# Kernel optimization log

Measured on AMD Instinct MI355X. Metric: run time of the kernel, lower is better.

Reference implementation:

```python
import jax, jax.numpy as jnp
import numpy as np

B, N, H, E = 8, 256, 128, 32

def setup_inputs() -> dict:
    key = jax.random.key(0)
    ks = jax.random.split(key, 9)
    x = jax.random.normal(ks[0], (B, N, H), dtype=jnp.float32)
    adj = jax.random.randint(ks[1], (B, N, N), 0, 2, dtype=jnp.int32)
    e = jax.random.normal(ks[2], (B, N, N, E), dtype=jnp.float32)
    s = 0.02
    We = jax.random.normal(ks[3], (E, H), dtype=jnp.float32) * s
    be = jax.random.normal(ks[4], (H,), dtype=jnp.float32) * s
    W1 = jax.random.normal(ks[5], (H, 2 * H), dtype=jnp.float32) * s
    b1 = jax.random.normal(ks[6], (2 * H,), dtype=jnp.float32) * s
    W2 = jax.random.normal(ks[7], (2 * H, H), dtype=jnp.float32) * s
    b2 = jax.random.normal(ks[8], (H,), dtype=jnp.float32) * s
    return {"x": x, "adj": adj, "e": e, "We": We, "be": be,
            "W1": W1, "b1": b1, "W2": W2, "b2": b2}

def reference(x, adj, e, We, be, W1, b1, W2, b2):
    # edge projection: [B,N,N,E] -> [B,N,N,H]
    e_h = jnp.einsum('bije,eh->bijh', e, We) + be
    # message m[b,i,j] = relu(x[b,j] + e_h[b,i,j]); mask by adj
    m = jax.nn.relu(x[:, None, :, :] + e_h)
    m = jnp.where((adj != 0)[..., None], m, jnp.zeros((), m.dtype))
    agg = m.sum(axis=2)  # sum over j -> [B,N,H]
    h = agg + x
    out = jax.nn.relu(h @ W1 + b1) @ W2 + b2
    return out
```

## Files before the change

### kernel.cpp

```cpp
#include <hip/hip_runtime.h>
#include <hip/hip_bf16.h>

#define B_ 8
#define N_ 256
#define H_ 128
#define E_ 32

typedef __bf16 bf16x8 __attribute__((ext_vector_type(8)));
typedef float f32x4 __attribute__((ext_vector_type(4)));

static __device__ __forceinline__ __bf16 f2bf(float f) {
    union { float f; unsigned int u; } a;
    a.f = f;
    const unsigned int r = a.u + 0x7FFFu + ((a.u >> 16) & 1u);
    union { unsigned short s; __bf16 b; } o;
    o.s = (unsigned short)(r >> 16);
    return o.b;
}

__global__ __launch_bounds__(256, 2) void fused_kernel(
    const float* __restrict__ x, const int* __restrict__ adj,
    const float* __restrict__ e, const float* __restrict__ We,
    const float* __restrict__ be, const float* __restrict__ W1,
    const float* __restrict__ b1, const float* __restrict__ W2,
    const float* __restrict__ b2, float* __restrict__ out)
{
    __shared__ float red[4][128];
    __shared__ float hvec[128];
    __shared__ float ts[256];
    __shared__ float part[256];

    const int bi   = blockIdx.x;
    const int b    = bi >> 8;
    const int tid  = threadIdx.x;
    const int w    = tid >> 6;
    const int lane = tid & 63;
    const int quad = lane >> 4;
    const int col  = lane & 15;

    bf16x8 bw[8];
    float  bef[8];
#pragma unroll
    for (int ht = 0; ht < 8; ++ht) {
#pragma unroll
        for (int kk = 0; kk < 8; ++kk)
            bw[ht][kk] = f2bf(We[(quad * 8 + kk) * H_ + ht * 16 + col]);
        bef[ht] = be[ht * 16 + col];
    }

    float psum[8];
#pragma unroll
    for (int ht = 0; ht < 8; ++ht) psum[ht] = 0.0f;

    const size_t ebase   = (size_t)bi * (N_ * E_);
    const size_t adjbase = (size_t)bi * N_;
    const f32x4 zero4 = {0.0f, 0.0f, 0.0f, 0.0f};

#pragma unroll
    for (int c = 0; c < 4; ++c) {
        const int j0 = (c * 4 + w) * 16;

        const float* ap = e + ebase + (size_t)(j0 + col) * E_ + quad * 8;
        const float4 a0 = *(const float4*)ap;
        const float4 a1 = *(const float4*)(ap + 4);
        bf16x8 af;
        af[0] = f2bf(a0.x); af[1] = f2bf(a0.y); af[2] = f2bf(a0.z); af[3] = f2bf(a0.w);
        af[4] = f2bf(a1.x); af[5] = f2bf(a1.y); af[6] = f2bf(a1.z); af[7] = f2bf(a1.w);

        float adjf[4];
        const int jr = j0 + quad * 4;
#pragma unroll
        for (int r = 0; r < 4; ++r)
            adjf[r] = adj[adjbase + jr + r] ? 1.0f : 0.0f;

        const float* xrow = x + ((size_t)(b * N_ + jr)) * H_ + col;

#pragma unroll
        for (int g = 0; g < 2; ++g) {
            f32x4 acc[4];
#pragma unroll
            for (int t = 0; t < 4; ++t)
                acc[t] = __builtin_amdgcn_mfma_f32_16x16x32_bf16(af, bw[g * 4 + t], zero4, 0, 0, 0);
#pragma unroll
            for (int r = 0; r < 4; ++r) {
                const float* xr = xrow + (size_t)r * H_;
#pragma unroll
                for (int t = 0; t < 4; ++t) {
                    const int ht = g * 4 + t;
                    const float v = acc[t][r] + xr[ht * 16] + bef[ht];
                    psum[ht] += adjf[r] * fmaxf(v, 0.0f);
                }
            }
        }
    }

#pragma unroll
    for (int ht = 0; ht < 8; ++ht) {
        float v = psum[ht];
        v += __shfl_xor(v, 16);
        v += __shfl_xor(v, 32);
        if (lane < 16) red[w][ht * 16 + lane] = v;
    }
    __syncthreads();
    if (tid < 128) {
        const float aggv = red[0][tid] + red[1][tid] + red[2][tid] + red[3][tid];
        hvec[tid] = aggv + x[(size_t)bi * H_ + tid];
    }
    __syncthreads();

    {
        const int c = tid;
        float a0 = 0.f, a1 = 0.f, a2 = 0.f, a3 = 0.f;
        for (int k = 0; k < 128; k += 4) {
            a0 += hvec[k + 0] * W1[(k + 0) * 256 + c];
            a1 += hvec[k + 1] * W1[(k + 1) * 256 + c];
            a2 += hvec[k + 2] * W1[(k + 2) * 256 + c];
            a3 += hvec[k + 3] * W1[(k + 3) * 256 + c];
        }
        ts[c] = fmaxf((a0 + a1) + (a2 + a3) + b1[c], 0.0f);
    }
    __syncthreads();

    {
        const int c    = tid & 127;
        const int kb   = (tid >> 7) * 128;
        float a0 = 0.f, a1 = 0.f, a2 = 0.f, a3 = 0.f;
        for (int k = 0; k < 128; k += 4) {
            a0 += ts[kb + k + 0] * W2[(kb + k + 0) * 128 + c];
            a1 += ts[kb + k + 1] * W2[(kb + k + 1) * 128 + c];
            a2 += ts[kb + k + 2] * W2[(kb + k + 2) * 128 + c];
            a3 += ts[kb + k + 3] * W2[(kb + k + 3) * 128 + c];
        }
        part[tid] = (a0 + a1) + (a2 + a3);
    }
    __syncthreads();
    if (tid < 128)
        out[(size_t)bi * H_ + tid] = part[tid] + part[tid + 128] + b2[tid];
}

extern "C" void kernel_launch(void* const* d_in, const int* in_sizes, int n_in,
                              void* d_out, int out_size, void* d_ws, size_t ws_size,
                              hipStream_t stream) {
    const float* x   = (const float*)d_in[0];
    const int*   adj = (const int*)  d_in[1];
    const float* e   = (const float*)d_in[2];
    const float* We  = (const float*)d_in[3];
    const float* be  = (const float*)d_in[4];
    const float* W1  = (const float*)d_in[5];
    const float* b1  = (const float*)d_in[6];
    const float* W2  = (const float*)d_in[7];
    const float* b2  = (const float*)d_in[8];
    float* out = (float*)d_out;

    fused_kernel<<<dim3(B_ * N_), dim3(256), 0, stream>>>(
        x, adj, e, We, be, W1, b1, W2, b2, out);
}
```

Measured before the change: 167.0 us.

## Process four nodes per block, stage x tiles in LDS, batch MLP

```diff
diff --git a/kernel.cpp b/kernel.cpp
--- a/kernel.cpp
+++ b/kernel.cpp
@@ -5,6 +5,7 @@
 #define N_ 256
 #define H_ 128
 #define E_ 32
+#define XS_STRIDE 132
 
 typedef __bf16 bf16x8 __attribute__((ext_vector_type(8)));
 typedef float f32x4 __attribute__((ext_vector_type(4)));
@@ -25,13 +26,15 @@
     const float* __restrict__ b1, const float* __restrict__ W2,
     const float* __restrict__ b2, float* __restrict__ out)
 {
-    __shared__ float red[4][128];
-    __shared__ float hvec[128];
-    __shared__ float ts[256];
-    __shared__ float part[256];
-
-    const int bi   = blockIdx.x;
-    const int b    = bi >> 8;
+    __shared__ float xs[4][16 * XS_STRIDE];
+    __shared__ float red[4][2][128];
+    __shared__ float hvec[4][128];
+    __shared__ float ts[4][256];
+    __shared__ float part[4][256];
+
+    const int tile = blockIdx.x;
+    const int b    = tile >> 6;
+    const int i0   = (tile & 63) << 2;
     const int tid  = threadIdx.x;
     const int w    = tid >> 6;
     const int lane = tid & 63;
@@ -48,94 +51,141 @@
         bef[ht] = be[ht * 16 + col];
     }
 
-    float psum[8];
-#pragma unroll
-    for (int ht = 0; ht < 8; ++ht) psum[ht] = 0.0f;
-
-    const size_t ebase   = (size_t)bi * (N_ * E_);
-    const size_t adjbase = (size_t)bi * N_;
     const f32x4 zero4 = {0.0f, 0.0f, 0.0f, 0.0f};
 
-#pragma unroll
-    for (int c = 0; c < 4; ++c) {
-        const int j0 = (c * 4 + w) * 16;
-
-        const float* ap = e + ebase + (size_t)(j0 + col) * E_ + quad * 8;
-        const float4 a0 = *(const float4*)ap;
-        const float4 a1 = *(const float4*)(ap + 4);
-        bf16x8 af;
-        af[0] = f2bf(a0.x); af[1] = f2bf(a0.y); af[2] = f2bf(a0.z); af[3] = f2bf(a0.w);
-        af[4] = f2bf(a1.x); af[5] = f2bf(a1.y); af[6] = f2bf(a1.z); af[7] = f2bf(a1.w);
-
-        float adjf[4];
-        const int jr = j0 + quad * 4;
-#pragma unroll
-        for (int r = 0; r < 4; ++r)
-            adjf[r] = adj[adjbase + jr + r] ? 1.0f : 0.0f;
-
-        const float* xrow = x + ((size_t)(b * N_ + jr)) * H_ + col;
-
-#pragma unroll
-        for (int g = 0; g < 2; ++g) {
-            f32x4 acc[4];
-#pragma unroll
-            for (int t = 0; t < 4; ++t)
-                acc[t] = __builtin_amdgcn_mfma_f32_16x16x32_bf16(af, bw[g * 4 + t], zero4, 0, 0, 0);
-#pragma unroll
-            for (int r = 0; r < 4; ++r) {
-                const float* xr = xrow + (size_t)r * H_;
-#pragma unroll
-                for (int t = 0; t < 4; ++t) {
-                    const int ht = g * 4 + t;
-                    const float v = acc[t][r] + xr[ht * 16] + bef[ht];
-                    psum[ht] += adjf[r] * fmaxf(v, 0.0f);
+    for (int pass = 0; pass < 2; ++pass) {
+        const int ia = i0 + pass * 2;
+
+        float psum[2][8];
+#pragma unroll
+        for (int ii = 0; ii < 2; ++ii)
+#pragma unroll
+            for (int ht = 0; ht < 8; ++ht) psum[ii][ht] = 0.0f;
+
+#pragma unroll
+        for (int c = 0; c < 4; ++c) {
+            const int j0 = (c * 4 + w) * 16;
+
+            {
+                const float* src = x + ((size_t)(b * N_ + j0)) * H_;
+#pragma unroll
+                for (int q = 0; q < 8; ++q) {
+                    const int idx = q * 64 + lane;
+                    const int row = idx >> 5, c4 = idx & 31;
+                    const float4 v = *(const float4*)(src + (size_t)idx * 4);
+                    *(float4*)&xs[w][row * XS_STRIDE + c4 * 4] = v;
                 }
             }
-        }
-    }
-
-#pragma unroll
-    for (int ht = 0; ht < 8; ++ht) {
-        float v = psum[ht];
-        v += __shfl_xor(v, 16);
-        v += __shfl_xor(v, 32);
-        if (lane < 16) red[w][ht * 16 + lane] = v;
-    }
-    __syncthreads();
-    if (tid < 128) {
-        const float aggv = red[0][tid] + red[1][tid] + red[2][tid] + red[3][tid];
-        hvec[tid] = aggv + x[(size_t)bi * H_ + tid];
-    }
-    __syncthreads();
+
+            const int jr = j0 + quad * 4;
+
+#pragma unroll
+            for (int ii = 0; ii < 2; ++ii) {
+                const int i = ia + ii;
+                const size_t rowbase = (size_t)(b * N_ + i) * N_;
+
+                const int4 av = *(const int4*)(adj + rowbase + jr);
+                float adjf[4];
+                adjf[0] = av.x ? 1.0f : 0.0f;
+                adjf[1] = av.y ? 1.0f : 0.0f;
+                adjf[2] = av.z ? 1.0f : 0.0f;
+                adjf[3] = av.w ? 1.0f : 0.0f;
+
+                const float* ap = e + (rowbase + (size_t)(j0 + col)) * E_ + quad * 8;
+                const float4 a0 = *(const float4*)ap;
+                const float4 a1 = *(const float4*)(ap + 4);
+                bf16x8 af;
+                af[0] = f2bf(a0.x); af[1] = f2bf(a0.y); af[2] = f2bf(a0.z); af[3] = f2bf(a0.w);
+                af[4] = f2bf(a1.x); af[5] = f2bf(a1.y); af[6] = f2bf(a1.z); af[7] = f2bf(a1.w);
+
+#pragma unroll
+                for (int g = 0; g < 2; ++g) {
+                    f32x4 acc[4];
+#pragma unroll
+                    for (int t = 0; t < 4; ++t)
+                        acc[t] = __builtin_amdgcn_mfma_f32_16x16x32_bf16(af, bw[g * 4 + t], zero4, 0, 0, 0);
+#pragma unroll
+                    for (int r = 0; r < 4; ++r) {
+                        const float* xr = &xs[w][(quad * 4 + r) * XS_STRIDE + col];
+#pragma unroll
+                        for (int t = 0; t < 4; ++t) {
+                            const int ht = g * 4 + t;
+                            const float v = acc[t][r] + xr[ht * 16] + bef[ht];
+                            psum[ii][ht] += adjf[r] * fmaxf(v, 0.0f);
+                        }
+                    }
+                }
+            }
+        }
+
+#pragma unroll
+        for (int ii = 0; ii < 2; ++ii)
+#pragma unroll
+            for (int ht = 0; ht < 8; ++ht) {
+                float v = psum[ii][ht];
+                v += __shfl_xor(v, 16);
+                v += __shfl_xor(v, 32);
+                if (lane < 16) red[w][ii][ht * 16 + lane] = v;
+            }
+        __syncthreads();
+        {
+            const int g = tid >> 7, t = tid & 127;
+            const float aggv = red[0][g][t] + red[1][g][t] + red[2][g][t] + red[3][g][t];
+            hvec[pass * 2 + g][t] = aggv + x[((size_t)(b * N_ + ia + g)) * H_ + t];
+        }
+        __syncthreads();
+    }
 
     {
         const int c = tid;
-        float a0 = 0.f, a1 = 0.f, a2 = 0.f, a3 = 0.f;
+        float acc[4] = {0.f, 0.f, 0.f, 0.f};
         for (int k = 0; k < 128; k += 4) {
-            a0 += hvec[k + 0] * W1[(k + 0) * 256 + c];
-            a1 += hvec[k + 1] * W1[(k + 1) * 256 + c];
-            a2 += hvec[k + 2] * W1[(k + 2) * 256 + c];
-            a3 += hvec[k + 3] * W1[(k + 3) * 256 + c];
-        }
-        ts[c] = fmaxf((a0 + a1) + (a2 + a3) + b1[c], 0.0f);
+            const float w0 = W1[(k + 0) * 256 + c];
+            const float w1 = W1[(k + 1) * 256 + c];
+            const float w2 = W1[(k + 2) * 256 + c];
+            const float w3 = W1[(k + 3) * 256 + c];
+#pragma unroll
+            for (int r = 0; r < 4; ++r) {
+                const float4 hv = *(const float4*)&hvec[r][k];
+                acc[r] += hv.x * w0 + hv.y * w1 + hv.z * w2 + hv.w * w3;
+            }
+        }
+        const float bb = b1[c];
+#pragma unroll
+        for (int r = 0; r < 4; ++r) ts[r][c] = fmaxf(acc[r] + bb, 0.0f);
     }
     __syncthreads();
 
     {
-        const int c    = tid & 127;
-        const int kb   = (tid >> 7) * 128;
-        float a0 = 0.f, a1 = 0.f, a2 = 0.f, a3 = 0.f;
+        const int cc = tid & 127;
+        const int kb = (tid >> 7) * 128;
+        float acc[4] = {0.f, 0.f, 0.f, 0.f};
         for (int k = 0; k < 128; k += 4) {
-            a0 += ts[kb + k + 0] * W2[(kb + k + 0) * 128 + c];
-            a1 += ts[kb + k + 1] * W2[(kb + k + 1) * 128 + c];
-            a2 += ts[kb + k + 2] * W2[(kb + k + 2) * 128 + c];
-            a3 += ts[kb + k + 3] * W2[(kb + k + 3) * 128 + c];
-        }
-        part[tid] = (a0 + a1) + (a2 + a3);
+            const float w0 = W2[(kb + k + 0) * 128 + cc];
+            const float w1 = W2[(kb + k + 1) * 128 + cc];
+            const float w2 = W2[(kb + k + 2) * 128 + cc];
+            const float w3 = W2[(kb + k + 3) * 128 + cc];
+#pragma unroll
+            for (int r = 0; r < 4; ++r) {
+                const float4 tv = *(const float4*)&ts[r][kb + k];
+                acc[r] += tv.x * w0 + tv.y * w1 + tv.z * w2 + tv.w * w3;
+            }
+        }
+#pragma unroll
+        for (int r = 0; r < 4; ++r) part[r][tid] = acc[r];
     }
     __syncthreads();
-    if (tid < 128)
-        out[(size_t)bi * H_ + tid] = part[tid] + part[tid + 128] + b2[tid];
+    {
+        const int t  = tid & 127;
+        const int rb = (tid >> 7) * 2;
+        const float bb = b2[t];
+#pragma unroll
+        for (int r2 = 0; r2 < 2; ++r2) {
+            const int r = rb + r2;
+            out[((size_t)(b * N_ + i0 + r)) * H_ + t] =
+                part[r][t] + part[r][t + 128] + bb;
+        }
+    }
 }
 
 extern "C" void kernel_launch(void* const* d_in, const int* in_sizes, int n_in,
@@ -152,6 +202,6 @@
     const float* b2  = (const float*)d_in[8];
     float* out = (float*)d_out;
 
-    fused_kernel<<<dim3(B_ * N_), dim3(256), 0, stream>>>(
+    fused_kernel<<<dim3(B_ * N_ / 4), dim3(256), 0, stream>>>(
         x, adj, e, We, be, W1, b1, W2, b2, out);
 }
```

After: 300.0 us. 1.8x slower.

## Process two node rows per block and stage edge weights in shared memory

Applied to the files above, without the earlier changes.

```diff
diff --git a/kernel.cpp b/kernel.cpp
--- a/kernel.cpp
+++ b/kernel.cpp
@@ -18,124 +18,154 @@
     return o.b;
 }
 
-__global__ __launch_bounds__(256, 2) void fused_kernel(
+__global__ __launch_bounds__(256, 3) void fused_kernel(
     const float* __restrict__ x, const int* __restrict__ adj,
     const float* __restrict__ e, const float* __restrict__ We,
     const float* __restrict__ be, const float* __restrict__ W1,
     const float* __restrict__ b1, const float* __restrict__ W2,
     const float* __restrict__ b2, float* __restrict__ out)
 {
+    __shared__ __bf16 wef[4 * 128 * 8];
     __shared__ float red[4][128];
-    __shared__ float hvec[128];
-    __shared__ float ts[256];
-    __shared__ float part[256];
+    __shared__ float hvec[2][128];
+    __shared__ float ts[2][256];
+    __shared__ float part[2][256];
 
-    const int bi   = blockIdx.x;
-    const int b    = bi >> 8;
+    const int tile = blockIdx.x;
+    const int b    = tile >> 7;
+    const int i0   = (tile & 127) << 1;
     const int tid  = threadIdx.x;
     const int w    = tid >> 6;
     const int lane = tid & 63;
     const int quad = lane >> 4;
     const int col  = lane & 15;
 
-    bf16x8 bw[8];
-    float  bef[8];
-#pragma unroll
-    for (int ht = 0; ht < 8; ++ht) {
+    for (int p = tid; p < 512; p += 256) {
+        const int q = p >> 7, hcol = p & 127;
+        bf16x8 t;
 #pragma unroll
         for (int kk = 0; kk < 8; ++kk)
-            bw[ht][kk] = f2bf(We[(quad * 8 + kk) * H_ + ht * 16 + col]);
-        bef[ht] = be[ht * 16 + col];
+            t[kk] = f2bf(We[(q * 8 + kk) * H_ + hcol]);
+        *(bf16x8*)&wef[p * 8] = t;
     }
+    __syncthreads();
 
-    float psum[8];
+    float bef[8];
 #pragma unroll
-    for (int ht = 0; ht < 8; ++ht) psum[ht] = 0.0f;
+    for (int ht = 0; ht < 8; ++ht) bef[ht] = be[ht * 16 + col];
 
-    const size_t ebase   = (size_t)bi * (N_ * E_);
-    const size_t adjbase = (size_t)bi * N_;
     const f32x4 zero4 = {0.0f, 0.0f, 0.0f, 0.0f};
 
+#pragma unroll 1
+    for (int ii = 0; ii < 2; ++ii) {
+        const int i = i0 + ii;
+        const size_t rowbase = (size_t)(b * N_ + i) * N_;
+
+        float psum[8];
 #pragma unroll
-    for (int c = 0; c < 4; ++c) {
-        const int j0 = (c * 4 + w) * 16;
-
-        const float* ap = e + ebase + (size_t)(j0 + col) * E_ + quad * 8;
-        const float4 a0 = *(const float4*)ap;
-        const float4 a1 = *(const float4*)(ap + 4);
-        bf16x8 af;
-        af[0] = f2bf(a0.x); af[1] = f2bf(a0.y); af[2] = f2bf(a0.z); af[3] = f2bf(a0.w);
-        af[4] = f2bf(a1.x); af[5] = f2bf(a1.y); af[6] = f2bf(a1.z); af[7] = f2bf(a1.w);
-
-        float adjf[4];
-        const int jr = j0 + quad * 4;
-#pragma unroll
-        for (int r = 0; r < 4; ++r)
-            adjf[r] = adj[adjbase + jr + r] ? 1.0f : 0.0f;
-
-        const float* xrow = x + ((size_t)(b * N_ + jr)) * H_ + col;
+        for (int ht = 0; ht < 8; ++ht) psum[ht] = 0.0f;
 
 #pragma unroll
-        for (int g = 0; g < 2; ++g) {
-            f32x4 acc[4];
+        for (int c = 0; c < 4; ++c) {
+            const int j0 = (c * 4 + w) * 16;
+            const int jr = j0 + quad * 4;
+
+            const int4 av = *(const int4*)(adj + rowbase + jr);
+            float adjf[4];
+            adjf[0] = av.x ? 1.0f : 0.0f;
+            adjf[1] = av.y ? 1.0f : 0.0f;
+            adjf[2] = av.z ? 1.0f : 0.0f;
+            adjf[3] = av.w ? 1.0f : 0.0f;
+
+            const float* ap = e + (rowbase + (size_t)(j0 + col)) * E_ + quad * 8;
+            const float4 a0 = *(const float4*)ap;
+            const float4 a1 = *(const float4*)(ap + 4);
+            bf16x8 af;
+            af[0] = f2bf(a0.x); af[1] = f2bf(a0.y); af[2] = f2bf(a0.z); af[3] = f2bf(a0.w);
+            af[4] = f2bf(a1.x); af[5] = f2bf(a1.y); af[6] = f2bf(a1.z); af[7] = f2bf(a1.w);
+
+            const float* xrow = x + ((size_t)(b * N_ + jr)) * H_ + col;
+
 #pragma unroll
-            for (int t = 0; t < 4; ++t)
-                acc[t] = __builtin_amdgcn_mfma_f32_16x16x32_bf16(af, bw[g * 4 + t], zero4, 0, 0, 0);
-#pragma unroll
-            for (int r = 0; r < 4; ++r) {
-                const float* xr = xrow + (size_t)r * H_;
+            for (int g = 0; g < 2; ++g) {
+                f32x4 acc[4];
 #pragma unroll
                 for (int t = 0; t < 4; ++t) {
-                    const int ht = g * 4 + t;
-                    const float v = acc[t][r] + xr[ht * 16] + bef[ht];
-                    psum[ht] += adjf[r] * fmaxf(v, 0.0f);
+                    const bf16x8 bwf =
+                        *(const bf16x8*)&wef[(quad * 128 + (g * 4 + t) * 16 + col) * 8];
+                    acc[t] = __builtin_amdgcn_mfma_f32_16x16x32_bf16(af, bwf, zero4, 0, 0, 0);
+                }
+#pragma unroll
+                for (int r = 0; r < 4; ++r) {
+                    const float* xr = xrow + (size_t)r * H_;
+#pragma unroll
+                    for (int t = 0; t < 4; ++t) {
+                        const int ht = g * 4 + t;
+                        const float v = acc[t][r] + xr[ht * 16] + bef[ht];
+                        psum[ht] += adjf[r] * fmaxf(v, 0.0f);
+                    }
                 }
             }
         }
+
+#pragma unroll
+        for (int ht = 0; ht < 8; ++ht) {
+            float v = psum[ht];
+            v += __shfl_xor(v, 16);
+            v += __shfl_xor(v, 32);
+            if (lane < 16) red[w][ht * 16 + lane] = v;
+        }
+        __syncthreads();
+        if (tid < 128) {
+            const float aggv = red[0][tid] + red[1][tid] + red[2][tid] + red[3][tid];
+            hvec[ii][tid] = aggv + x[((size_t)(b * N_ + i)) * H_ + tid];
+        }
+        __syncthreads();
     }
 
-#pragma unroll
-    for (int ht = 0; ht < 8; ++ht) {
-        float v = psum[ht];
-        v += __shfl_xor(v, 16);
-        v += __shfl_xor(v, 32);
-        if (lane < 16) red[w][ht * 16 + lane] = v;
-    }
-    __syncthreads();
-    if (tid < 128) {
-        const float aggv = red[0][tid] + red[1][tid] + red[2][tid] + red[3][tid];
-        hvec[tid] = aggv + x[(size_t)bi * H_ + tid];
+    {
+        const int c = tid;
+        float acc0 = 0.f, acc1 = 0.f;
+        for (int k = 0; k < 128; k += 4) {
+            const float w0 = W1[(k + 0) * 256 + c];
+            const float w1 = W1[(k + 1) * 256 + c];
+            const float w2 = W1[(k + 2) * 256 + c];
+            const float w3 = W1[(k + 3) * 256 + c];
+            const float4 h0 = *(const float4*)&hvec[0][k];
+            const float4 h1 = *(const float4*)&hvec[1][k];
+            acc0 += h0.x * w0 + h0.y * w1 + h0.z * w2 + h0.w * w3;
+            acc1 += h1.x * w0 + h1.y * w1 + h1.z * w2 + h1.w * w3;
+        }
+        const float bb = b1[c];
+        ts[0][c] = fmaxf(acc0 + bb, 0.0f);
+        ts[1][c] = fmaxf(acc1 + bb, 0.0f);
     }
     __syncthreads();
 
     {
-        const int c = tid;
-        float a0 = 0.f, a1 = 0.f, a2 = 0.f, a3 = 0.f;
+        const int cc = tid & 127;
+        const int kb = (tid >> 7) * 128;
+        float acc0 = 0.f, acc1 = 0.f;
         for (int k = 0; k < 128; k += 4) {
-            a0 += hvec[k + 0] * W1[(k + 0) * 256 + c];
-            a1 += hvec[k + 1] * W1[(k + 1) * 256 + c];
-            a2 += hvec[k + 2] * W1[(k + 2) * 256 + c];
-            a3 += hvec[k + 3] * W1[(k + 3) * 256 + c];
+            const float w0 = W2[(kb + k + 0) * 128 + cc];
+            const float w1 = W2[(kb + k + 1) * 128 + cc];
+            const float w2 = W2[(kb + k + 2) * 128 + cc];
+            const float w3 = W2[(kb + k + 3) * 128 + cc];
+            const float4 t0 = *(const float4*)&ts[0][kb + k];
+            const float4 t1 = *(const float4*)&ts[1][kb + k];
+            acc0 += t0.x * w0 + t0.y * w1 + t0.z * w2 + t0.w * w3;
+            acc1 += t1.x * w0 + t1.y * w1 + t1.z * w2 + t1.w * w3;
         }
-        ts[c] = fmaxf((a0 + a1) + (a2 + a3) + b1[c], 0.0f);
+        part[0][tid] = acc0;
+        part[1][tid] = acc1;
     }
     __syncthreads();
-
     {
-        const int c    = tid & 127;
-        const int kb   = (tid >> 7) * 128;
-        float a0 = 0.f, a1 = 0.f, a2 = 0.f, a3 = 0.f;
-        for (int k = 0; k < 128; k += 4) {
-            a0 += ts[kb + k + 0] * W2[(kb + k + 0) * 128 + c];
-            a1 += ts[kb + k + 1] * W2[(kb + k + 1) * 128 + c];
-            a2 += ts[kb + k + 2] * W2[(kb + k + 2) * 128 + c];
-            a3 += ts[kb + k + 3] * W2[(kb + k + 3) * 128 + c];
-        }
-        part[tid] = (a0 + a1) + (a2 + a3);
+        const int t = tid & 127;
+        const int r = tid >> 7;
+        out[((size_t)(b * N_ + i0 + r)) * H_ + t] =
+            part[r][t] + part[r][t + 128] + b2[t];
     }
-    __syncthreads();
-    if (tid < 128)
-        out[(size_t)bi * H_ + tid] = part[tid] + part[tid + 128] + b2[tid];
 }
 
 extern "C" void kernel_launch(void* const* d_in, const int* in_sizes, int n_in,
@@ -152,6 +182,6 @@
     const float* b2  = (const float*)d_in[8];
     float* out = (float*)d_out;
 
-    fused_kernel<<<dim3(B_ * N_), dim3(256), 0, stream>>>(
+    fused_kernel<<<dim3(B_ * N_ / 2), dim3(256), 0, stream>>>(
         x, adj, e, We, be, W1, b1, W2, b2, out);
 }
```

Measured after the change: 343.0 us. 2.05x slower.

## Prefetch next edge chunk, vectorize adj loads, and prefold bias into x

Applied to the files above, without the earlier changes.

```diff
diff --git a/kernel.cpp b/kernel.cpp
--- a/kernel.cpp
+++ b/kernel.cpp
@@ -18,10 +18,21 @@
     return o.b;
 }
 
+__global__ __launch_bounds__(256) void xb_kernel(
+    const float* __restrict__ x, const float* __restrict__ be,
+    float* __restrict__ xb)
+{
+    const int idx = blockIdx.x * 256 + threadIdx.x;
+    float4 v = ((const float4*)x)[idx];
+    const float4 bv = ((const float4*)be)[idx & 31];
+    v.x += bv.x; v.y += bv.y; v.z += bv.z; v.w += bv.w;
+    ((float4*)xb)[idx] = v;
+}
+
 __global__ __launch_bounds__(256, 2) void fused_kernel(
     const float* __restrict__ x, const int* __restrict__ adj,
     const float* __restrict__ e, const float* __restrict__ We,
-    const float* __restrict__ be, const float* __restrict__ W1,
+    const float* __restrict__ xb, const float* __restrict__ W1,
     const float* __restrict__ b1, const float* __restrict__ W2,
     const float* __restrict__ b2, float* __restrict__ out)
 {
@@ -39,14 +50,11 @@
     const int col  = lane & 15;
 
     bf16x8 bw[8];
-    float  bef[8];
 #pragma unroll
-    for (int ht = 0; ht < 8; ++ht) {
+    for (int ht = 0; ht < 8; ++ht)
 #pragma unroll
         for (int kk = 0; kk < 8; ++kk)
             bw[ht][kk] = f2bf(We[(quad * 8 + kk) * H_ + ht * 16 + col]);
-        bef[ht] = be[ht * 16 + col];
-    }
 
     float psum[8];
 #pragma unroll
@@ -56,24 +64,39 @@
     const size_t adjbase = (size_t)bi * N_;
     const f32x4 zero4 = {0.0f, 0.0f, 0.0f, 0.0f};
 
+    float4 a0, a1;
+    int4   av;
+    {
+        const int j0 = w * 16;
+        const float* ap = e + ebase + (size_t)(j0 + col) * E_ + quad * 8;
+        a0 = *(const float4*)ap;
+        a1 = *(const float4*)(ap + 4);
+        av = *(const int4*)(adj + adjbase + j0 + quad * 4);
+    }
+
 #pragma unroll
     for (int c = 0; c < 4; ++c) {
         const int j0 = (c * 4 + w) * 16;
+        const int jr = j0 + quad * 4;
 
-        const float* ap = e + ebase + (size_t)(j0 + col) * E_ + quad * 8;
-        const float4 a0 = *(const float4*)ap;
-        const float4 a1 = *(const float4*)(ap + 4);
         bf16x8 af;
         af[0] = f2bf(a0.x); af[1] = f2bf(a0.y); af[2] = f2bf(a0.z); af[3] = f2bf(a0.w);
         af[4] = f2bf(a1.x); af[5] = f2bf(a1.y); af[6] = f2bf(a1.z); af[7] = f2bf(a1.w);
+        float adjf[4];
+        adjf[0] = av.x ? 1.0f : 0.0f;
+        adjf[1] = av.y ? 1.0f : 0.0f;
+        adjf[2] = av.z ? 1.0f : 0.0f;
+        adjf[3] = av.w ? 1.0f : 0.0f;
 
-        float adjf[4];
-        const int jr = j0 + quad * 4;
-#pragma unroll
-        for (int r = 0; r < 4; ++r)
-            adjf[r] = adj[adjbase + jr + r] ? 1.0f : 0.0f;
+        if (c < 3) {
+            const int j0n = ((c + 1) * 4 + w) * 16;
+            const float* apn = e + ebase + (size_t)(j0n + col) * E_ + quad * 8;
+            a0 = *(const float4*)apn;
+            a1 = *(const float4*)(apn + 4);
+            av = *(const int4*)(adj + adjbase + j0n + quad * 4);
+        }
 
-        const float* xrow = x + ((size_t)(b * N_ + jr)) * H_ + col;
+        const float* xbrow = xb + ((size_t)(b * N_ + jr)) * H_ + col;
 
 #pragma unroll
         for (int g = 0; g < 2; ++g) {
@@ -83,11 +106,11 @@
                 acc[t] = __builtin_amdgcn_mfma_f32_16x16x32_bf16(af, bw[g * 4 + t], zero4, 0, 0, 0);
 #pragma unroll
             for (int r = 0; r < 4; ++r) {
-                const float* xr = xrow + (size_t)r * H_;
+                const float* xr = xbrow + (size_t)r * H_;
 #pragma unroll
                 for (int t = 0; t < 4; ++t) {
                     const int ht = g * 4 + t;
-                    const float v = acc[t][r] + xr[ht * 16] + bef[ht];
+                    const float v = acc[t][r] + xr[ht * 16];
                     psum[ht] += adjf[r] * fmaxf(v, 0.0f);
                 }
             }
@@ -110,28 +133,28 @@
 
     {
         const int c = tid;
-        float a0 = 0.f, a1 = 0.f, a2 = 0.f, a3 = 0.f;
+        float a0m = 0.f, a1m = 0.f, a2m = 0.f, a3m = 0.f;
         for (int k = 0; k < 128; k += 4) {
-            a0 += hvec[k + 0] * W1[(k + 0) * 256 + c];
-            a1 += hvec[k + 1] * W1[(k + 1) * 256 + c];
-            a2 += hvec[k + 2] * W1[(k + 2) * 256 + c];
-            a3 += hvec[k + 3] * W1[(k + 3) * 256 + c];
+            a0m += hvec[k + 0] * W1[(k + 0) * 256 + c];
+            a1m += hvec[k + 1] * W1[(k + 1) * 256 + c];
+            a2m += hvec[k + 2] * W1[(k + 2) * 256 + c];
+            a3m += hvec[k + 3] * W1[(k + 3) * 256 + c];
         }
-        ts[c] = fmaxf((a0 + a1) + (a2 + a3) + b1[c], 0.0f);
+        ts[c] = fmaxf((a0m + a1m) + (a2m + a3m) + b1[c], 0.0f);
     }
     __syncthreads();
 
     {
-        const int c    = tid & 127;
-        const int kb   = (tid >> 7) * 128;
-        float a0 = 0.f, a1 = 0.f, a2 = 0.f, a3 = 0.f;
+        const int c  = tid & 127;
+        const int kb = (tid >> 7) * 128;
+        float a0m = 0.f, a1m = 0.f, a2m = 0.f, a3m = 0.f;
         for (int k = 0; k < 128; k += 4) {
-            a0 += ts[kb + k + 0] * W2[(kb + k + 0) * 128 + c];
-            a1 += ts[kb + k + 1] * W2[(kb + k + 1) * 128 + c];
-            a2 += ts[kb + k + 2] * W2[(kb + k + 2) * 128 + c];
-            a3 += ts[kb + k + 3] * W2[(kb + k + 3) * 128 + c];
+            a0m += ts[kb + k + 0] * W2[(kb + k + 0) * 128 + c];
+            a1m += ts[kb + k + 1] * W2[(kb + k + 1) * 128 + c];
+            a2m += ts[kb + k + 2] * W2[(kb + k + 2) * 128 + c];
+            a3m += ts[kb + k + 3] * W2[(kb + k + 3) * 128 + c];
         }
-        part[tid] = (a0 + a1) + (a2 + a3);
+        part[tid] = (a0m + a1m) + (a2m + a3m);
     }
     __syncthreads();
     if (tid < 128)
@@ -151,7 +174,9 @@
     const float* W2  = (const float*)d_in[7];
     const float* b2  = (const float*)d_in[8];
     float* out = (float*)d_out;
+    float* xbw = (float*)d_ws;
 
+    xb_kernel<<<dim3(B_ * N_ * H_ / 1024), dim3(256), 0, stream>>>(x, be, xbw);
     fused_kernel<<<dim3(B_ * N_), dim3(256), 0, stream>>>(
-        x, adj, e, We, be, W1, b1, W2, b2, out);
+        x, adj, e, We, xbw, W1, b1, W2, b2, out);
 }
```

Result: no change. 169.1 us (+1.2%).
